# Performance work log

Hardware: AMD Instinct MI355X
Metric: run time of the kernel (lower is better)

The kernel has to match this reference:

```python
import jax, jax.numpy as jnp
import numpy as np

EPS = 1e-12  # torch F.normalize clamp_min eps

def _l2_normalize(x):
    n = jnp.linalg.norm(x, axis=-1, keepdims=True)
    return x / jnp.maximum(n, EPS)

def setup_inputs() -> dict:
    key = jax.random.key(0)
    k1, k2 = jax.random.split(key)
    z_e = jax.random.normal(k1, (32, 256, 32, 32), dtype=jnp.float32)
    weight = jax.random.normal(k2, (1024, 256), dtype=jnp.float32)
    return {"z_e": z_e, "weight": weight}

def reference(z_e, weight):
    B, C, H, W = z_e.shape  # C == embedding_dim
    z = jnp.transpose(z_e, (0, 2, 3, 1))            # [B,H,W,C]
    flat = _l2_normalize(z.reshape(-1, C))          # [N,C]
    w_n = _l2_normalize(weight)                     # [K,C]
    # distances = 2 - 2 * <flat, w_n>; computed without grad in original
    dist = 2.0 - 2.0 * jnp.matmul(flat, w_n.T)      # [N,K]
    idx = jnp.argmin(dist, axis=1)                  # [N]
    z_q = w_n[idx].reshape(B, H, W, C)              # gather codebook rows
    z_q = jnp.transpose(z_q, (0, 3, 1, 2))          # [B,C,H,W]
    indices = idx.reshape(B, H, W)
    return z_q, indices
```

## Files before the change

### kernel.cpp

```cpp
#include <hip/hip_runtime.h>


typedef _Float16 half8 __attribute__((ext_vector_type(8)));
typedef _Float16 half4 __attribute__((ext_vector_type(4)));
typedef float    floatx4 __attribute__((ext_vector_type(4)));
typedef float    floatv4 __attribute__((ext_vector_type(4)));

#define C_DIM 256
#define K_CODES 1024
#define HW 1024
#define NPIX 32768
#define USTR 520

#define GLOAD_LDS16(g, l) __builtin_amdgcn_global_load_lds(                    \
    (const __attribute__((address_space(1))) unsigned int*)(g),                \
    (__attribute__((address_space(3))) unsigned int*)(l), 16, 0, 0)

__global__ __launch_bounds__(256) void vq_norm_w(const float* __restrict__ w,
                                                 float* __restrict__ w_nT,
                                                 _Float16* __restrict__ wh,
                                                 _Float16* __restrict__ wl) {
    const int row = blockIdx.x;
    const int t   = threadIdx.x;
    float x = w[row * C_DIM + t];
    float s = x * x;
    #pragma unroll
    for (int off = 32; off > 0; off >>= 1) s += __shfl_down(s, off, 64);
    __shared__ float wsum[4];
    if ((t & 63) == 0) wsum[t >> 6] = s;
    __syncthreads();
    float tot = wsum[0] + wsum[1] + wsum[2] + wsum[3];
    float inv = 1.0f / fmaxf(sqrtf(tot), 1e-12f);
    float y = x * inv;
    w_nT[t * K_CODES + row] = y;
    float ys = 16.0f * y;
    _Float16 hi = (_Float16)ys;
    wh[row * C_DIM + t] = hi;
    wl[row * C_DIM + t] = (_Float16)(ys - (float)hi);
}

__global__ __launch_bounds__(256, 4) void vq_gemm(
        const float* __restrict__ z,
        const _Float16* __restrict__ wh, const _Float16* __restrict__ wl,
        float* __restrict__ cand_val, int* __restrict__ cand_idx) {
    __shared__ _Float16 Ah[8 * USTR], Al[8 * USTR];
    __shared__ _Float16 Bh[8 * USTR], Bl[8 * USTR];
    __shared__ float red_v[128][2];
    __shared__ int   red_i[128][2];

    const int tid  = threadIdx.x;
    const int lane = tid & 63, wave = tid >> 6;
    const int wm = wave >> 1, wn = wave & 1;
    const int quad = lane >> 4, l15 = lane & 15;
    const int m0 = blockIdx.x * 128, n0 = blockIdx.y * 128;
    const int b  = m0 >> 10, p0 = m0 & 1023;

    const _Float16* bsrc = (wave < 2) ? wh : wl;
    _Float16*       bdst = (wave < 2) ? Bh : Bl;
    const int ub = (wave & 1) * 4;
    const _Float16* gB[4];
    _Float16*       lB[4];
    #pragma unroll
    for (int i = 0; i < 4; i++) {
        gB[i] = bsrc + (size_t)(n0 + (ub + i) * 16 + l15) * C_DIM + quad * 8;
        lB[i] = bdst + (ub + i) * USTR;
    }

    const int ap = (lane & 31) * 4;
    const int as = lane >> 5;
    const int ak = wave * 8 + as * 4;
    const float* zA = z + ((size_t)b * C_DIM + ak) * HW + p0 + ap;

    floatx4 acc[4][4];
    #pragma unroll
    for (int i = 0; i < 4; i++)
        #pragma unroll
        for (int j = 0; j < 4; j++) acc[i][j] = (floatx4){0.f, 0.f, 0.f, 0.f};

    const int afrag = wm * 4, bfrag = wn * 4;

    for (int kt = 0; kt < 8; kt++) {
        __syncthreads();
        #pragma unroll
        for (int i = 0; i < 4; i++)
            GLOAD_LDS16(gB[i] + kt * 32, lB[i]);
        floatv4 za[4];
        #pragma unroll
        for (int r = 0; r < 4; r++)
            za[r] = *(const floatv4*)(zA + (size_t)(kt * 32 + r) * HW);
        #pragma unroll
        for (int i = 0; i < 4; i++) {
            half4 hv, lv;
            #pragma unroll
            for (int r = 0; r < 4; r++) {
                float xv = 4.0f * za[r][i];
                _Float16 h = (_Float16)xv;
                hv[r] = h;
                lv[r] = (_Float16)(xv - (float)h);
            }
            const int p = ap + i;
            const int aidx = (p >> 4) * USTR + wave * 128 + (p & 15) * 8 + as * 4;
            *(half4*)&Ah[aidx] = hv;
            *(half4*)&Al[aidx] = lv;
        }
        __syncthreads();

        half8 ah[4], al[4], bh[4], bl[4];
        #pragma unroll
        for (int i = 0; i < 4; i++) {
            ah[i] = *(const half8*)&Ah[(afrag + i) * USTR + lane * 8];
            al[i] = *(const half8*)&Al[(afrag + i) * USTR + lane * 8];
            bh[i] = *(const half8*)&Bh[(bfrag + i) * USTR + lane * 8];
            bl[i] = *(const half8*)&Bl[(bfrag + i) * USTR + lane * 8];
        }
        #pragma unroll
        for (int mi = 0; mi < 4; mi++)
            #pragma unroll
            for (int ni = 0; ni < 4; ni++) {
                acc[mi][ni] = __builtin_amdgcn_mfma_f32_16x16x32_f16(ah[mi], bh[ni], acc[mi][ni], 0, 0, 0);
                acc[mi][ni] = __builtin_amdgcn_mfma_f32_16x16x32_f16(ah[mi], bl[ni], acc[mi][ni], 0, 0, 0);
                acc[mi][ni] = __builtin_amdgcn_mfma_f32_16x16x32_f16(al[mi], bh[ni], acc[mi][ni], 0, 0, 0);
            }
    }

    #pragma unroll
    for (int mi = 0; mi < 4; mi++) {
        #pragma unroll
        for (int r = 0; r < 4; r++) {
            float bv = -__builtin_inff();
            int   bi = 0x7fffffff;
            #pragma unroll
            for (int ni = 0; ni < 4; ni++) {
                float v = acc[mi][ni][r];
                int  ci = n0 + wn * 64 + ni * 16 + l15;
                if (v > bv || (v == bv && ci < bi)) { bv = v; bi = ci; }
            }
            #pragma unroll
            for (int mk = 8; mk; mk >>= 1) {
                float ov = __shfl_xor(bv, mk, 16);
                int   oi = __shfl_xor(bi, mk, 16);
                if (ov > bv || (ov == bv && oi < bi)) { bv = ov; bi = oi; }
            }
            if (l15 == 0) {
                int row = wm * 64 + mi * 16 + quad * 4 + r;
                red_v[row][wn] = bv;
                red_i[row][wn] = bi;
            }
        }
    }
    __syncthreads();
    if (tid < 128) {
        float bv = red_v[tid][0]; int bi = red_i[tid][0];
        float v2 = red_v[tid][1]; int i2 = red_i[tid][1];
        if (v2 > bv || (v2 == bv && i2 < bi)) { bv = v2; bi = i2; }
        const int pix = m0 + tid;
        cand_val[(size_t)pix * 8 + blockIdx.y] = bv;
        cand_idx[(size_t)pix * 8 + blockIdx.y] = bi;
    }
}

__global__ __launch_bounds__(256) void vq_finalize(
        const float* __restrict__ cand_val,
        const int*   __restrict__ cand_idx,
        const float* __restrict__ w_nT,
        float* __restrict__ zq,
        float* __restrict__ idx_out) {
    __shared__ int idx_s[1024];
    const int t  = threadIdx.x;
    const int b  = blockIdx.x;
    const int cg = blockIdx.y;
    #pragma unroll
    for (int q = 0; q < 4; q++) {
        const int p = q * 256 + t;
        const int n = b * 1024 + p;
        const size_t base = (size_t)n * 8;
        float bv = cand_val[base]; int bi = cand_idx[base];
        #pragma unroll
        for (int j = 1; j < 8; j++) {
            float v = cand_val[base + j];
            int   c = cand_idx[base + j];
            if (v > bv || (v == bv && c < bi)) { bv = v; bi = c; }
        }
        idx_s[p] = bi;
        if (cg == 0) idx_out[n] = (float)bi;
    }
    __syncthreads();
    float* zqb = zq + (size_t)b * (C_DIM * HW);
    for (int c = 0; c < 32; c++) {
        const int ch = cg * 32 + c;
        const float* wrow = w_nT + (size_t)ch * K_CODES;
        #pragma unroll
        for (int q = 0; q < 4; q++) {
            const int p = q * 256 + t;
            zqb[(size_t)ch * HW + p] = wrow[idx_s[p]];
        }
    }
}

extern "C" void kernel_launch(void* const* d_in, const int* in_sizes, int n_in,
                              void* d_out, int out_size, void* d_ws, size_t ws_size,
                              hipStream_t stream) {
    const float* z = (const float*)d_in[0];
    const float* w = (const float*)d_in[1];
    float* out     = (float*)d_out;

    char* ws = (char*)d_ws;
    float*    w_nT = (float*)(ws);
    _Float16* wh   = (_Float16*)(ws + (1u << 20));
    _Float16* wl   = (_Float16*)(ws + (3u << 19));
    float*    cval = (float*)(ws + (2u << 20));
    int*      cidx = (int*)(ws + (3u << 20));

    vq_norm_w<<<K_CODES, 256, 0, stream>>>(w, w_nT, wh, wl);
    vq_gemm<<<dim3(NPIX / 128, K_CODES / 128), 256, 0, stream>>>(z, wh, wl, cval, cidx);
    vq_finalize<<<dim3(32, 8), 256, 0, stream>>>(cval, cidx, w_nT, out, out + 8388608);
}
```

Baseline: 175.4 us.

## Pre-swizzle codebook into MFMA fragment layout and double-buffer A tile

The normalization kernel now writes the split-fp16 codebook directly in the per-lane MFMA fragment order, so the GEMM loads B fragments straight from global memory into registers and no longer stages B through LDS. The A tile (converted z) is double-buffered in LDS: the next k-slice is loaded from global before the MFMAs and converted and stored after them, which leaves one barrier per iteration. This is meant to hide global latency and cut LDS traffic and synchronisation, at the cost of more registers (launch bounds drop from 4 to 3 waves per SIMD) and redundant global B reads across the two wm waves.

New measurement: 186.2 us. +6.2%, slower.

```diff
diff --git a/kernel.cpp b/kernel.cpp
--- a/kernel.cpp
+++ b/kernel.cpp
@@ -4,22 +4,18 @@
 typedef _Float16 half8 __attribute__((ext_vector_type(8)));
 typedef _Float16 half4 __attribute__((ext_vector_type(4)));
 typedef float    floatx4 __attribute__((ext_vector_type(4)));
-typedef float    floatv4 __attribute__((ext_vector_type(4)));
 
 #define C_DIM 256
 #define K_CODES 1024
 #define HW 1024
 #define NPIX 32768
+#define NTILES 8
 #define USTR 520
-
-#define GLOAD_LDS16(g, l) __builtin_amdgcn_global_load_lds(                    \
-    (const __attribute__((address_space(1))) unsigned int*)(g),                \
-    (__attribute__((address_space(3))) unsigned int*)(l), 16, 0, 0)
 
 __global__ __launch_bounds__(256) void vq_norm_w(const float* __restrict__ w,
                                                  float* __restrict__ w_nT,
-                                                 _Float16* __restrict__ wh,
-                                                 _Float16* __restrict__ wl) {
+                                                 _Float16* __restrict__ whF,
+                                                 _Float16* __restrict__ wlF) {
     const int row = blockIdx.x;
     const int t   = threadIdx.x;
     float x = w[row * C_DIM + t];
@@ -35,16 +31,18 @@
     w_nT[t * K_CODES + row] = y;
     float ys = 16.0f * y;
     _Float16 hi = (_Float16)ys;
-    wh[row * C_DIM + t] = hi;
-    wl[row * C_DIM + t] = (_Float16)(ys - (float)hi);
-}
-
-__global__ __launch_bounds__(256, 4) void vq_gemm(
+    const int gu = row >> 4, l15 = row & 15;
+    const int kt = t >> 5, quad = (t >> 3) & 3, j = t & 7;
+    const int idx = (kt * 64 + gu) * 512 + (quad * 16 + l15) * 8 + j;
+    whF[idx] = hi;
+    wlF[idx] = (_Float16)(ys - (float)hi);
+}
+
+__global__ __launch_bounds__(256, 3) void vq_gemm(
         const float* __restrict__ z,
-        const _Float16* __restrict__ wh, const _Float16* __restrict__ wl,
+        const _Float16* __restrict__ whF, const _Float16* __restrict__ wlF,
         float* __restrict__ cand_val, int* __restrict__ cand_idx) {
-    __shared__ _Float16 Ah[8 * USTR], Al[8 * USTR];
-    __shared__ _Float16 Bh[8 * USTR], Bl[8 * USTR];
+    __shared__ _Float16 A[2][2][8 * USTR];
     __shared__ float red_v[128][2];
     __shared__ int   red_i[128][2];
 
@@ -55,21 +53,13 @@
     const int m0 = blockIdx.x * 128, n0 = blockIdx.y * 128;
     const int b  = m0 >> 10, p0 = m0 & 1023;
 
-    const _Float16* bsrc = (wave < 2) ? wh : wl;
-    _Float16*       bdst = (wave < 2) ? Bh : Bl;
-    const int ub = (wave & 1) * 4;
-    const _Float16* gB[4];
-    _Float16*       lB[4];
-    #pragma unroll
-    for (int i = 0; i < 4; i++) {
-        gB[i] = bsrc + (size_t)(n0 + (ub + i) * 16 + l15) * C_DIM + quad * 8;
-        lB[i] = bdst + (ub + i) * USTR;
-    }
-
     const int ap = (lane & 31) * 4;
     const int as = lane >> 5;
     const int ak = wave * 8 + as * 4;
     const float* zA = z + ((size_t)b * C_DIM + ak) * HW + p0 + ap;
+    const int aidx0 = (ap >> 4) * USTR + wave * 128 + (ap & 15) * 8 + as * 4;
+
+    const int gu0 = blockIdx.y * 8 + wn * 4;
 
     floatx4 acc[4][4];
     #pragma unroll
@@ -77,17 +67,13 @@
         #pragma unroll
         for (int j = 0; j < 4; j++) acc[i][j] = (floatx4){0.f, 0.f, 0.f, 0.f};
 
-    const int afrag = wm * 4, bfrag = wn * 4;
-
-    for (int kt = 0; kt < 8; kt++) {
-        __syncthreads();
-        #pragma unroll
-        for (int i = 0; i < 4; i++)
-            GLOAD_LDS16(gB[i] + kt * 32, lB[i]);
-        floatv4 za[4];
+    const int afrag = wm * 4;
+
+    {
+        floatx4 za[4];
         #pragma unroll
         for (int r = 0; r < 4; r++)
-            za[r] = *(const floatv4*)(zA + (size_t)(kt * 32 + r) * HW);
+            za[r] = *(const floatx4*)(zA + (size_t)r * HW);
         #pragma unroll
         for (int i = 0; i < 4; i++) {
             half4 hv, lv;
@@ -98,21 +84,36 @@
                 hv[r] = h;
                 lv[r] = (_Float16)(xv - (float)h);
             }
-            const int p = ap + i;
-            const int aidx = (p >> 4) * USTR + wave * 128 + (p & 15) * 8 + as * 4;
-            *(half4*)&Ah[aidx] = hv;
-            *(half4*)&Al[aidx] = lv;
-        }
+            const int aidx = aidx0 + ((i >> 2) ? 0 : 0) + ((((ap + i) >> 4) - (ap >> 4)) * USTR) + (((ap + i) & 15) - (ap & 15)) * 8;
+            *(half4*)&A[0][0][aidx] = hv;
+            *(half4*)&A[0][1][aidx] = lv;
+        }
+    }
+
+    for (int kt = 0; kt < 8; kt++) {
         __syncthreads();
-
-        half8 ah[4], al[4], bh[4], bl[4];
+        const int cb = kt & 1;
+
+        half8 bh[4], bl[4];
         #pragma unroll
         for (int i = 0; i < 4; i++) {
-            ah[i] = *(const half8*)&Ah[(afrag + i) * USTR + lane * 8];
-            al[i] = *(const half8*)&Al[(afrag + i) * USTR + lane * 8];
-            bh[i] = *(const half8*)&Bh[(bfrag + i) * USTR + lane * 8];
-            bl[i] = *(const half8*)&Bl[(bfrag + i) * USTR + lane * 8];
-        }
+            const size_t bidx = (size_t)(kt * 64 + gu0 + i) * 512 + lane * 8;
+            bh[i] = *(const half8*)(whF + bidx);
+            bl[i] = *(const half8*)(wlF + bidx);
+        }
+        half8 ah[4], al[4];
+        #pragma unroll
+        for (int i = 0; i < 4; i++) {
+            ah[i] = *(const half8*)&A[cb][0][(afrag + i) * USTR + lane * 8];
+            al[i] = *(const half8*)&A[cb][1][(afrag + i) * USTR + lane * 8];
+        }
+        floatx4 zan[4];
+        if (kt < 7) {
+            #pragma unroll
+            for (int r = 0; r < 4; r++)
+                zan[r] = *(const floatx4*)(zA + (size_t)((kt + 1) * 32 + r) * HW);
+        }
+
         #pragma unroll
         for (int mi = 0; mi < 4; mi++)
             #pragma unroll
@@ -121,6 +122,25 @@
                 acc[mi][ni] = __builtin_amdgcn_mfma_f32_16x16x32_f16(ah[mi], bl[ni], acc[mi][ni], 0, 0, 0);
                 acc[mi][ni] = __builtin_amdgcn_mfma_f32_16x16x32_f16(al[mi], bh[ni], acc[mi][ni], 0, 0, 0);
             }
+
+        if (kt < 7) {
+            const int nb = cb ^ 1;
+            #pragma unroll
+            for (int i = 0; i < 4; i++) {
+                half4 hv, lv;
+                #pragma unroll
+                for (int r = 0; r < 4; r++) {
+                    float xv = 4.0f * zan[r][i];
+                    _Float16 h = (_Float16)xv;
+                    hv[r] = h;
+                    lv[r] = (_Float16)(xv - (float)h);
+                }
+                const int p = ap + i;
+                const int aidx = (p >> 4) * USTR + wave * 128 + (p & 15) * 8 + as * 4;
+                *(half4*)&A[nb][0][aidx] = hv;
+                *(half4*)&A[nb][1][aidx] = lv;
+            }
+        }
     }
 
     #pragma unroll
@@ -132,7 +152,7 @@
             #pragma unroll
             for (int ni = 0; ni < 4; ni++) {
                 float v = acc[mi][ni][r];
-                int  ci = n0 + wn * 64 + ni * 16 + l15;
+                int  ci = n0 + (wn * 4 + ni) * 16 + l15;
                 if (v > bv || (v == bv && ci < bi)) { bv = v; bi = ci; }
             }
             #pragma unroll
@@ -154,8 +174,8 @@
         float v2 = red_v[tid][1]; int i2 = red_i[tid][1];
         if (v2 > bv || (v2 == bv && i2 < bi)) { bv = v2; bi = i2; }
         const int pix = m0 + tid;
-        cand_val[(size_t)pix * 8 + blockIdx.y] = bv;
-        cand_idx[(size_t)pix * 8 + blockIdx.y] = bi;
+        cand_val[(size_t)pix * NTILES + blockIdx.y] = bv;
+        cand_idx[(size_t)pix * NTILES + blockIdx.y] = bi;
     }
 }
 
@@ -173,10 +193,10 @@
     for (int q = 0; q < 4; q++) {
         const int p = q * 256 + t;
         const int n = b * 1024 + p;
-        const size_t base = (size_t)n * 8;
+        const size_t base = (size_t)n * NTILES;
         float bv = cand_val[base]; int bi = cand_idx[base];
         #pragma unroll
-        for (int j = 1; j < 8; j++) {
+        for (int j = 1; j < NTILES; j++) {
             float v = cand_val[base + j];
             int   c = cand_idx[base + j];
             if (v > bv || (v == bv && c < bi)) { bv = v; bi = c; }
@@ -206,12 +226,12 @@
 
     char* ws = (char*)d_ws;
     float*    w_nT = (float*)(ws);
-    _Float16* wh   = (_Float16*)(ws + (1u << 20));
-    _Float16* wl   = (_Float16*)(ws + (3u << 19));
+    _Float16* whF  = (_Float16*)(ws + (1u << 20));
+    _Float16* wlF  = (_Float16*)(ws + (3u << 19));
     float*    cval = (float*)(ws + (2u << 20));
     int*      cidx = (int*)(ws + (3u << 20));
 
-    vq_norm_w<<<K_CODES, 256, 0, stream>>>(w, w_nT, wh, wl);
-    vq_gemm<<<dim3(NPIX / 128, K_CODES / 128), 256, 0, stream>>>(z, wh, wl, cval, cidx);
+    vq_norm_w<<<K_CODES, 256, 0, stream>>>(w, w_nT, whF, wlF);
+    vq_gemm<<<dim3(NPIX / 128, NTILES), 256, 0, stream>>>(z, whF, wlF, cval, cidx);
     vq_finalize<<<dim3(32, 8), 256, 0, stream>>>(cval, cidx, w_nT, out, out + 8388608);
 }
```

## Gather codebook rows into LDS tile and transpose for coalesced finalize

Applied to the files above, without the earlier changes.

Stores the normalized codebook row-major instead of transposed, and rewrites the finalize kernel so each block handles 64 pixels. Each block gathers whole codebook rows with vector loads into a padded LDS tile, then writes the NCHW output with float4 stores. This replaces scattered per-element gathers from the transposed codebook across a 256-block grid with coalesced row reads. The cost is an LDS transpose with strided column reads and a larger grid that needs more LDS per block.

Result: faster. 155.9 us (-11.2%).

```diff
diff --git a/kernel.cpp b/kernel.cpp
--- a/kernel.cpp
+++ b/kernel.cpp
@@ -4,12 +4,12 @@
 typedef _Float16 half8 __attribute__((ext_vector_type(8)));
 typedef _Float16 half4 __attribute__((ext_vector_type(4)));
 typedef float    floatx4 __attribute__((ext_vector_type(4)));
-typedef float    floatv4 __attribute__((ext_vector_type(4)));
 
 #define C_DIM 256
 #define K_CODES 1024
 #define HW 1024
 #define NPIX 32768
+#define NTILES 8
 #define USTR 520
 
 #define GLOAD_LDS16(g, l) __builtin_amdgcn_global_load_lds(                    \
@@ -17,7 +17,7 @@
     (__attribute__((address_space(3))) unsigned int*)(l), 16, 0, 0)
 
 __global__ __launch_bounds__(256) void vq_norm_w(const float* __restrict__ w,
-                                                 float* __restrict__ w_nT,
+                                                 float* __restrict__ w_n,
                                                  _Float16* __restrict__ wh,
                                                  _Float16* __restrict__ wl) {
     const int row = blockIdx.x;
@@ -32,7 +32,7 @@
     float tot = wsum[0] + wsum[1] + wsum[2] + wsum[3];
     float inv = 1.0f / fmaxf(sqrtf(tot), 1e-12f);
     float y = x * inv;
-    w_nT[t * K_CODES + row] = y;
+    w_n[row * C_DIM + t] = y;
     float ys = 16.0f * y;
     _Float16 hi = (_Float16)ys;
     wh[row * C_DIM + t] = hi;
@@ -84,10 +84,10 @@
         #pragma unroll
         for (int i = 0; i < 4; i++)
             GLOAD_LDS16(gB[i] + kt * 32, lB[i]);
-        floatv4 za[4];
+        floatx4 za[4];
         #pragma unroll
         for (int r = 0; r < 4; r++)
-            za[r] = *(const floatv4*)(zA + (size_t)(kt * 32 + r) * HW);
+            za[r] = *(const floatx4*)(zA + (size_t)(kt * 32 + r) * HW);
         #pragma unroll
         for (int i = 0; i < 4; i++) {
             half4 hv, lv;
@@ -154,46 +154,53 @@
         float v2 = red_v[tid][1]; int i2 = red_i[tid][1];
         if (v2 > bv || (v2 == bv && i2 < bi)) { bv = v2; bi = i2; }
         const int pix = m0 + tid;
-        cand_val[(size_t)pix * 8 + blockIdx.y] = bv;
-        cand_idx[(size_t)pix * 8 + blockIdx.y] = bi;
+        cand_val[(size_t)pix * NTILES + blockIdx.y] = bv;
+        cand_idx[(size_t)pix * NTILES + blockIdx.y] = bi;
     }
 }
 
 __global__ __launch_bounds__(256) void vq_finalize(
         const float* __restrict__ cand_val,
         const int*   __restrict__ cand_idx,
-        const float* __restrict__ w_nT,
+        const float* __restrict__ w_n,
         float* __restrict__ zq,
         float* __restrict__ idx_out) {
-    __shared__ int idx_s[1024];
-    const int t  = threadIdx.x;
-    const int b  = blockIdx.x;
-    const int cg = blockIdx.y;
-    #pragma unroll
-    for (int q = 0; q < 4; q++) {
-        const int p = q * 256 + t;
-        const int n = b * 1024 + p;
-        const size_t base = (size_t)n * 8;
+    __shared__ float tile[64][257];
+    __shared__ int   idx_s[64];
+    const int t    = threadIdx.x;
+    const int lane = t & 63, wave = t >> 6;
+    const int n0   = blockIdx.x * 64;
+    const int b    = n0 >> 10, p0 = n0 & 1023;
+
+    if (t < 64) {
+        const int n = n0 + t;
+        const size_t base = (size_t)n * NTILES;
         float bv = cand_val[base]; int bi = cand_idx[base];
         #pragma unroll
-        for (int j = 1; j < 8; j++) {
+        for (int j = 1; j < NTILES; j++) {
             float v = cand_val[base + j];
             int   c = cand_idx[base + j];
             if (v > bv || (v == bv && c < bi)) { bv = v; bi = c; }
         }
-        idx_s[p] = bi;
-        if (cg == 0) idx_out[n] = (float)bi;
-    }
-    __syncthreads();
-    float* zqb = zq + (size_t)b * (C_DIM * HW);
-    for (int c = 0; c < 32; c++) {
-        const int ch = cg * 32 + c;
-        const float* wrow = w_nT + (size_t)ch * K_CODES;
-        #pragma unroll
-        for (int q = 0; q < 4; q++) {
-            const int p = q * 256 + t;
-            zqb[(size_t)ch * HW + p] = wrow[idx_s[p]];
-        }
+        idx_s[t] = bi;
+        idx_out[n] = (float)bi;
+    }
+    __syncthreads();
+    #pragma unroll
+    for (int i = 0; i < 16; i++) {
+        const int p = wave * 16 + i;
+        const int row = idx_s[p];
+        floatx4 v = *(const floatx4*)(w_n + (size_t)row * C_DIM + lane * 4);
+        *(floatx4*)&tile[p][lane * 4] = v;
+    }
+    __syncthreads();
+    float* zqb = zq + (size_t)b * (C_DIM * HW) + p0;
+    #pragma unroll
+    for (int it = 0; it < 16; it++) {
+        const int c = it * 16 + wave * 4 + (lane >> 4);
+        const int p = (lane & 15) * 4;
+        floatx4 v = { tile[p][c], tile[p + 1][c], tile[p + 2][c], tile[p + 3][c] };
+        *(floatx4*)(zqb + (size_t)c * HW + p) = v;
     }
 }
 
@@ -205,13 +212,13 @@
     float* out     = (float*)d_out;
 
     char* ws = (char*)d_ws;
-    float*    w_nT = (float*)(ws);
+    float*    w_n  = (float*)(ws);
     _Float16* wh   = (_Float16*)(ws + (1u << 20));
     _Float16* wl   = (_Float16*)(ws + (3u << 19));
     float*    cval = (float*)(ws + (2u << 20));
     int*      cidx = (int*)(ws + (3u << 20));
 
-    vq_norm_w<<<K_CODES, 256, 0, stream>>>(w, w_nT, wh, wl);
-    vq_gemm<<<dim3(NPIX / 128, K_CODES / 128), 256, 0, stream>>>(z, wh, wl, cval, cidx);
-    vq_finalize<<<dim3(32, 8), 256, 0, stream>>>(cval, cidx, w_nT, out, out + 8388608);
-}
+    vq_norm_w<<<K_CODES, 256, 0, stream>>>(w, w_n, wh, wl);
+    vq_gemm<<<dim3(NPIX / 128, NTILES), 256, 0, stream>>>(z, wh, wl, cval, cidx);
+    vq_finalize<<<NPIX / 64, 256, 0, stream>>>(cval, cidx, w_n, out, out + 8388608);
+}
```
